# Kernel optimization log

Measured on AMD Instinct MI355X. Metric: run time of the kernel, lower is better.

Reference implementation:

```python
import jax, jax.numpy as jnp
import numpy as np

N, D, M, L, DEPTH, WIDTH, MPTS = 2048, 64, 2048, 16, 3, 128, 64
WIN = 2 * L + 1  # 33


def setup_inputs() -> dict:
    key = jax.random.key(0)
    ks = jax.random.split(key, 6)
    # xavier-normal-ish scales to keep sigmoids in a reasonable range
    s0 = float(np.sqrt(2.0 / (D + WIDTH)))
    s1 = float(np.sqrt(2.0 / (2 * WIDTH)))
    s2 = float(np.sqrt(2.0 / (WIDTH + WIN)))
    return {
        "u": jax.random.normal(ks[0], (MPTS, D), dtype=jnp.float32),
        "weight0": jax.random.normal(ks[1], (WIN, WIDTH, D), dtype=jnp.float32) * s0,
        "bias0": jnp.zeros((WIN, WIDTH, 1), dtype=jnp.float32),
        "weight": jax.random.normal(ks[2], (DEPTH - 1, WIN, WIDTH, WIDTH), dtype=jnp.float32) * s1,
        "bias": jnp.zeros((DEPTH - 1, WIN, WIDTH, 1), dtype=jnp.float32),
        "weight_final": jax.random.normal(ks[3], (M, WIN, WIDTH), dtype=jnp.float32) * s2,
        "bias_final": jnp.zeros((M, WIN, 1), dtype=jnp.float32),
        "xi": jax.random.normal(ks[4], (M, N + 2 * L), dtype=jnp.float32) * 0.1,
    }


def reference(u, weight0, bias0, weight, bias, weight_final, bias_final, xi):
    sig = jax.nn.sigmoid
    # first_step: shared per-frequency MLP stack
    u1 = sig(jnp.einsum('jkl,ml->jkm', weight0, u) + bias0)
    for i in range(weight.shape[0]):  # depth-1 hidden layers (small fixed count)
        u1 = sig(jnp.einsum('jkl,jlm->jkm', weight[i], u1) + bias[i])
    G = sig(jnp.einsum('ijk,jkm->ijm', weight_final, u1) + bias_final)
    # sliding-window weighted sum over spectral coeffs, vectorized as a 1D
    # cross-correlation: out[n, p] = sum_{m,j} xi[m, n+j] * G[m, j, p]
    kernel = jnp.transpose(G, (2, 0, 1))
    out = jax.lax.conv_general_dilated(
        xi[None],  # [1, M, N+2L]
        kernel,
        window_strides=(1,),
        padding='VALID',
        dimension_numbers=('NCH', 'OIH', 'NCH'),
    )  # [1, MPTS, N]
    return out[0].T  # [N, MPTS] == torch.cat over iter_prod
```

## Files before the change

### kernel.cpp

```cpp
#include <hip/hip_runtime.h>

#define WIN 33
#define WIDTH 128
#define MPTS 64
#define NN 2048
#define MM 2048
#define DD 64
#define NQ 2080

typedef __bf16 bf16x8 __attribute__((ext_vector_type(8)));
typedef float f32x4 __attribute__((ext_vector_type(4)));

__device__ __forceinline__ unsigned short f2bf(float x) {
  union { float f; unsigned int u; } v; v.f = x;
  unsigned int r = v.u + 0x7FFFu + ((v.u >> 16) & 1u);
  return (unsigned short)(r >> 16);
}
__device__ __forceinline__ float sigf(float x) { return 1.0f / (1.0f + __expf(-x)); }

__device__ __forceinline__ void gll16(const unsigned short* g, unsigned short* l) {
  __builtin_amdgcn_global_load_lds(
      (const __attribute__((address_space(1))) unsigned int*)g,
      (__attribute__((address_space(3))) unsigned int*)l, 16, 0, 0);
}

__global__ __launch_bounds__(256) void k_transpose(const float* __restrict__ xi,
                                                   unsigned short* __restrict__ xiT) {
  __shared__ float ts[64 * 37];
  int qb = blockIdx.x * 32;
  int mb = blockIdx.y * 64;
#pragma unroll
  for (int c = threadIdx.x; c < 512; c += 256) {
    int row = c >> 3, c8 = c & 7;
    float4 v = *(const float4*)&xi[(size_t)(mb + row) * NQ + qb + (c8 << 2)];
    ts[row * 37 + (c8 << 2) + 0] = v.x;
    ts[row * 37 + (c8 << 2) + 1] = v.y;
    ts[row * 37 + (c8 << 2) + 2] = v.z;
    ts[row * 37 + (c8 << 2) + 3] = v.w;
  }
  __syncthreads();
#pragma unroll
  for (int c = threadIdx.x; c < 512; c += 256) {
    int r = c >> 4, mq = c & 15;
    ushort4 h;
    h.x = f2bf(ts[(mq * 4 + 0) * 37 + r]);
    h.y = f2bf(ts[(mq * 4 + 1) * 37 + r]);
    h.z = f2bf(ts[(mq * 4 + 2) * 37 + r]);
    h.w = f2bf(ts[(mq * 4 + 3) * 37 + r]);
    *(ushort4*)&xiT[((size_t)blockIdx.y * NQ + (qb + r)) * 64 + (mq << 2)] = h;
  }
}

__global__ __launch_bounds__(256) void k_mlp(const float* __restrict__ u,
                                             const float* __restrict__ w0,
                                             const float* __restrict__ b0,
                                             const float* __restrict__ w,
                                             const float* __restrict__ bias,
                                             unsigned short* __restrict__ u1bf) {
  constexpr int WS = 72;
  constexpr int AS = 136;
  __shared__ unsigned short ws[128 * WS];
  __shared__ unsigned short actA[64 * AS];
  __shared__ unsigned short actB[64 * AS];
  __shared__ float biass[128];
  int j = blockIdx.x;
  int tid = threadIdx.x;
  int wv = tid >> 6, lane = tid & 63, l15 = lane & 15, l4 = lane >> 4;

#pragma unroll
  for (int c = tid; c < 1024; c += 256) {
    int p = c >> 4, d4 = (c & 15) << 2;
    float4 v = *(const float4*)&u[(size_t)p * DD + d4];
    ushort4 h; h.x = f2bf(v.x); h.y = f2bf(v.y); h.z = f2bf(v.z); h.w = f2bf(v.w);
    *(ushort4*)&actA[p * AS + d4] = h;
  }
#pragma unroll
  for (int c = tid; c < 2048; c += 256) {
    int k = c >> 4, d4 = (c & 15) << 2;
    float4 v = *(const float4*)&w0[((size_t)j * 128 + k) * DD + d4];
    ushort4 h; h.x = f2bf(v.x); h.y = f2bf(v.y); h.z = f2bf(v.z); h.w = f2bf(v.w);
    *(ushort4*)&ws[k * WS + d4] = h;
  }
  if (tid < 128) biass[tid] = b0[j * 128 + tid];
  __syncthreads();

  {
    f32x4 acc[2][4] = {};
#pragma unroll
    for (int t = 0; t < 2; ++t) {
      int col = (t << 5) + (l4 << 3);
      bf16x8 a[2], b[4];
#pragma unroll
      for (int s = 0; s < 2; ++s)
        a[s] = *(const bf16x8*)&ws[(wv * 32 + s * 16 + l15) * WS + col];
#pragma unroll
      for (int q = 0; q < 4; ++q)
        b[q] = *(const bf16x8*)&actA[(q * 16 + l15) * AS + col];
#pragma unroll
      for (int s = 0; s < 2; ++s)
#pragma unroll
        for (int q = 0; q < 4; ++q)
          acc[s][q] = __builtin_amdgcn_mfma_f32_16x16x32_bf16(a[s], b[q], acc[s][q], 0, 0, 0);
    }
#pragma unroll
    for (int s = 0; s < 2; ++s)
#pragma unroll
      for (int q = 0; q < 4; ++q) {
        int p = q * 16 + l15;
#pragma unroll
        for (int r = 0; r < 4; ++r) {
          int k = wv * 32 + s * 16 + (l4 << 2) + r;
          actB[p * AS + k] = f2bf(sigf(acc[s][q][r] + biass[k]));
        }
      }
  }

  unsigned short* ain = actB;
  unsigned short* aout = actA;
#pragma unroll
  for (int i = 0; i < 2; ++i) {
    f32x4 acc[2][4] = {};
    const float* wbase = w + ((size_t)i * WIN + j) * 128 * 128;
#pragma unroll
    for (int h = 0; h < 2; ++h) {
      __syncthreads();
#pragma unroll
      for (int c = tid; c < 2048; c += 256) {
        int k = c >> 4, d4 = (c & 15) << 2;
        float4 v = *(const float4*)&wbase[(size_t)k * 128 + h * 64 + d4];
        ushort4 hh; hh.x = f2bf(v.x); hh.y = f2bf(v.y); hh.z = f2bf(v.z); hh.w = f2bf(v.w);
        *(ushort4*)&ws[k * WS + d4] = hh;
      }
      if (h == 0 && tid < 128) biass[tid] = bias[((size_t)i * WIN + j) * 128 + tid];
      __syncthreads();
#pragma unroll
      for (int t = 0; t < 2; ++t) {
        int col = (t << 5) + (l4 << 3);
        bf16x8 a[2], b[4];
#pragma unroll
        for (int s = 0; s < 2; ++s)
          a[s] = *(const bf16x8*)&ws[(wv * 32 + s * 16 + l15) * WS + col];
#pragma unroll
        for (int q = 0; q < 4; ++q)
          b[q] = *(const bf16x8*)&ain[(q * 16 + l15) * AS + h * 64 + col];
#pragma unroll
        for (int s = 0; s < 2; ++s)
#pragma unroll
          for (int q = 0; q < 4; ++q)
            acc[s][q] = __builtin_amdgcn_mfma_f32_16x16x32_bf16(a[s], b[q], acc[s][q], 0, 0, 0);
      }
    }
#pragma unroll
    for (int s = 0; s < 2; ++s)
#pragma unroll
      for (int q = 0; q < 4; ++q) {
        int p = q * 16 + l15;
#pragma unroll
        for (int r = 0; r < 4; ++r) {
          int k = wv * 32 + s * 16 + (l4 << 2) + r;
          aout[p * AS + k] = f2bf(sigf(acc[s][q][r] + biass[k]));
        }
      }
    unsigned short* t2 = ain; ain = aout; aout = t2;
  }
  __syncthreads();
#pragma unroll
  for (int c = tid; c < 1024; c += 256) {
    int p = c >> 4, k8 = (c & 15) << 3;
    uint4 v = *(const uint4*)&ain[p * AS + k8];
    *(uint4*)&u1bf[((size_t)j * MPTS + p) * WIDTH + k8] = v;
  }
}

__global__ __launch_bounds__(256) void k_final(const float* __restrict__ wf,
                                               const float* __restrict__ bfin,
                                               const unsigned short* __restrict__ u1bf,
                                               unsigned short* __restrict__ Gt2) {
  constexpr int KP = 136;
  __shared__ unsigned short As[64 * KP];
  __shared__ unsigned short Bs[64 * KP];
  __shared__ float bfs[64];
  int bid = blockIdx.x;
  int j = bid >> 5;
  int m0 = (bid & 31) << 6;
#pragma unroll
  for (int c = threadIdx.x; c < 64 * 32; c += 256) {
    int row = c >> 5, f4 = c & 31;
    float4 v = *(const float4*)(wf + ((size_t)(m0 + row) * WIN + j) * WIDTH + (f4 << 2));
    ushort4 h;
    h.x = f2bf(v.x); h.y = f2bf(v.y); h.z = f2bf(v.z); h.w = f2bf(v.w);
    *(ushort4*)(&As[row * KP + (f4 << 2)]) = h;
  }
#pragma unroll
  for (int c = threadIdx.x; c < 64 * 16; c += 256) {
    int p = c >> 4, ch = c & 15;
    uint4 v = *(const uint4*)(u1bf + (size_t)(j * MPTS + p) * WIDTH + (ch << 3));
    *(uint4*)(&Bs[p * KP + (ch << 3)]) = v;
  }
  if (threadIdx.x < 64) bfs[threadIdx.x] = bfin[(size_t)(m0 + threadIdx.x) * WIN + j];
  __syncthreads();
  int wv = threadIdx.x >> 6, lane = threadIdx.x & 63;
  int l15 = lane & 15, l4 = lane >> 4;
  f32x4 acc[4] = {};
#pragma unroll
  for (int t = 0; t < 4; ++t) {
    int col = (t << 5) + (l4 << 3);
    bf16x8 a = *(const bf16x8*)(&As[(wv * 16 + l15) * KP + col]);
#pragma unroll
    for (int q = 0; q < 4; ++q) {
      bf16x8 bb = *(const bf16x8*)(&Bs[(q * 16 + l15) * KP + col]);
      acc[q] = __builtin_amdgcn_mfma_f32_16x16x32_bf16(a, bb, acc[q], 0, 0, 0);
    }
  }
  size_t region = (size_t)((bid & 31) << 1) + (wv >> 1);
  int g = ((wv & 1) << 1) + (l4 >> 1);
  int m8 = (l4 & 1) << 2;
  int mb = wv * 16 + (l4 << 2);
#pragma unroll
  for (int q = 0; q < 4; ++q) {
    int p = q * 16 + l15;
    float z0 = acc[q][0] + bfs[mb + 0];
    float z1 = acc[q][1] + bfs[mb + 1];
    float z2 = acc[q][2] + bfs[mb + 2];
    float z3 = acc[q][3] + bfs[mb + 3];
    ushort4 st;
    st.x = f2bf(sigf(z0)); st.y = f2bf(sigf(z1));
    st.z = f2bf(sigf(z2)); st.w = f2bf(sigf(z3));
    *(ushort4*)(&Gt2[region * 67584 + ((size_t)(j * 4 + g) * 64 + p) * 8 + m8]) = st;
  }
}

__global__ __launch_bounds__(256) void k_conv(const unsigned short* __restrict__ xiT,
                                              const unsigned short* __restrict__ Gt2,
                                              float* __restrict__ out) {
  extern __shared__ unsigned short lds[];
  unsigned short* As = lds;
  int bid = blockIdx.x;
  int mp = bid & 31;
  int n0 = (bid >> 5) << 7;
  int tid = threadIdx.x;
  int wv = tid >> 6, lane = tid & 63, l15 = lane & 15, l4 = lane >> 4;

  const unsigned short* Abase = xiT + (size_t)mp * (NQ * 64) + (size_t)n0 * 64;
#pragma unroll
  for (int k = 0; k < 5; ++k) {
    int instr = wv * 5 + k;
    int s = (instr << 6) + lane;
    int row = s >> 3;
    int c = (s & 7) ^ (row & 7);
    gll16(Abase + (size_t)row * 64 + (c << 3), As + (instr << 9));
  }

  constexpr int JBT[10]  = {0, 7, 14, 21, 28, 0, 7, 14, 21, 28};
  constexpr int CNTT[10] = {7, 7, 7, 7, 5, 7, 7, 7, 7, 5};
  constexpr int HFT[10]  = {0, 0, 0, 0, 0, 1, 1, 1, 1, 1};

  const unsigned short* Rb0 = Gt2 + (size_t)(mp << 1) * 67584;
  const unsigned short* Rb1 = Gt2 + (size_t)((mp << 1) + 1) * 67584;

  {
    const unsigned short* Bb = Rb0;
#pragma unroll
    for (int k = 0; k < 7; ++k) {
      int instr = wv * 7 + k;
      gll16(Bb + (((instr << 6) + lane) << 3), lds + 10240 + (instr << 9));
    }
  }

  f32x4 acc[2][4] = {};
#pragma unroll
  for (int t = 0; t < 10; ++t) {
    __syncthreads();
    if (t < 9) {
      const int jbn = JBT[t + 1], cntn = CNTT[t + 1];
      const unsigned short* Bb =
          (HFT[t + 1] ? Rb1 : Rb0) + ((size_t)jbn << 11);
      unsigned short* Bst = lds + 10240 + ((t + 1) & 1) * 14336;
#pragma unroll
      for (int k = 0; k < cntn; ++k) {
        int instr = wv * cntn + k;
        gll16(Bb + (((instr << 6) + lane) << 3), Bst + (instr << 9));
      }
    }
    {
      const int jb = JBT[t], cnt = CNTT[t], h4 = HFT[t] << 2;
      const unsigned short* Bs = lds + 10240 + (t & 1) * 14336;
      bf16x8 a[2], b[4];
#pragma unroll
      for (int s = 0; s < 2; ++s) {
        int row = wv * 32 + s * 16 + l15 + jb;
        a[s] = *(const bf16x8*)&As[row * 64 + (((h4 | l4) ^ (row & 7)) << 3)];
      }
#pragma unroll
      for (int q = 0; q < 4; ++q) {
        int slot = (l4 << 6) + (q << 4) + l15;
        b[q] = *(const bf16x8*)&Bs[slot << 3];
      }
#pragma unroll
      for (int jj = 0; jj < cnt; ++jj) {
        bf16x8 an[2], bn[4];
        if (jj < cnt - 1) {
#pragma unroll
          for (int s = 0; s < 2; ++s) {
            int row = wv * 32 + s * 16 + l15 + jb + jj + 1;
            an[s] = *(const bf16x8*)&As[row * 64 + (((h4 | l4) ^ (row & 7)) << 3)];
          }
#pragma unroll
          for (int q = 0; q < 4; ++q) {
            int slot = ((((jj + 1) << 2) + l4) << 6) + (q << 4) + l15;
            bn[q] = *(const bf16x8*)&Bs[slot << 3];
          }
        }
#pragma unroll
        for (int s = 0; s < 2; ++s)
#pragma unroll
          for (int q = 0; q < 4; ++q)
            acc[s][q] = __builtin_amdgcn_mfma_f32_16x16x32_bf16(a[s], b[q], acc[s][q], 0, 0, 0);
#pragma unroll
        for (int s = 0; s < 2; ++s) a[s] = an[s];
#pragma unroll
        for (int q = 0; q < 4; ++q) b[q] = bn[q];
      }
    }
  }
#pragma unroll
  for (int s = 0; s < 2; ++s)
#pragma unroll
    for (int q = 0; q < 4; ++q) {
      int nr = n0 + wv * 32 + s * 16 + (l4 << 2);
      int p = q * 16 + l15;
#pragma unroll
      for (int i = 0; i < 4; ++i)
        atomicAdd(&out[(size_t)(nr + i) * MPTS + p], acc[s][q][i]);
    }
}

extern "C" void kernel_launch(void* const* d_in, const int* in_sizes, int n_in,
                              void* d_out, int out_size, void* d_ws, size_t ws_size,
                              hipStream_t stream) {
  const float* u    = (const float*)d_in[0];
  const float* w0   = (const float*)d_in[1];
  const float* b0   = (const float*)d_in[2];
  const float* w    = (const float*)d_in[3];
  const float* bias = (const float*)d_in[4];
  const float* wf   = (const float*)d_in[5];
  const float* bfin = (const float*)d_in[6];
  const float* xi   = (const float*)d_in[7];
  float* out = (float*)d_out;
  char* ws = (char*)d_ws;
  unsigned short* xiT  = (unsigned short*)(ws);
  unsigned short* Gt2  = (unsigned short*)(ws + 8519680);
  unsigned short* u1bf = (unsigned short*)(ws + 17170432);

  hipFuncSetAttribute(reinterpret_cast<const void*>(&k_conv),
                      hipFuncAttributeMaxDynamicSharedMemorySize, 77824);

  hipMemsetAsync(out, 0, (size_t)out_size * sizeof(float), stream);
  k_transpose<<<dim3(65, 32), 256, 0, stream>>>(xi, xiT);
  k_mlp<<<WIN, 256, 0, stream>>>(u, w0, b0, w, bias, u1bf);
  k_final<<<33 * 32, 256, 0, stream>>>(wf, bfin, u1bf, Gt2);
  k_conv<<<512, 256, 77824, stream>>>(xiT, Gt2, out);
}
```

Measured before the change: 161.5 us.

## Fuse memset, xi transpose and MLP into one heterogeneous prep kernel

Replaces the output memset, the xi transpose kernel and the per-frequency MLP kernel with a single launch. Blocks 0-32 run the MLP, and the remaining blocks transpose xi to bf16 and zero the output. This removes two launch and serialization gaps and lets the small 33-block MLP overlap with the transpose work. In exchange, every block reserves the MLP's large dynamic shared memory, which may limit occupancy for the transpose blocks.

Result: faster. 153.3 us (-5.1%).

```diff
diff --git a/kernel.cpp b/kernel.cpp
--- a/kernel.cpp
+++ b/kernel.cpp
@@ -24,115 +24,48 @@
       (__attribute__((address_space(3))) unsigned int*)l, 16, 0, 0);
 }
 
-__global__ __launch_bounds__(256) void k_transpose(const float* __restrict__ xi,
-                                                   unsigned short* __restrict__ xiT) {
-  __shared__ float ts[64 * 37];
-  int qb = blockIdx.x * 32;
-  int mb = blockIdx.y * 64;
-#pragma unroll
-  for (int c = threadIdx.x; c < 512; c += 256) {
-    int row = c >> 3, c8 = c & 7;
-    float4 v = *(const float4*)&xi[(size_t)(mb + row) * NQ + qb + (c8 << 2)];
-    ts[row * 37 + (c8 << 2) + 0] = v.x;
-    ts[row * 37 + (c8 << 2) + 1] = v.y;
-    ts[row * 37 + (c8 << 2) + 2] = v.z;
-    ts[row * 37 + (c8 << 2) + 3] = v.w;
-  }
-  __syncthreads();
-#pragma unroll
-  for (int c = threadIdx.x; c < 512; c += 256) {
-    int r = c >> 4, mq = c & 15;
-    ushort4 h;
-    h.x = f2bf(ts[(mq * 4 + 0) * 37 + r]);
-    h.y = f2bf(ts[(mq * 4 + 1) * 37 + r]);
-    h.z = f2bf(ts[(mq * 4 + 2) * 37 + r]);
-    h.w = f2bf(ts[(mq * 4 + 3) * 37 + r]);
-    *(ushort4*)&xiT[((size_t)blockIdx.y * NQ + (qb + r)) * 64 + (mq << 2)] = h;
-  }
-}
-
-__global__ __launch_bounds__(256) void k_mlp(const float* __restrict__ u,
-                                             const float* __restrict__ w0,
-                                             const float* __restrict__ b0,
-                                             const float* __restrict__ w,
-                                             const float* __restrict__ bias,
-                                             unsigned short* __restrict__ u1bf) {
-  constexpr int WS = 72;
-  constexpr int AS = 136;
-  __shared__ unsigned short ws[128 * WS];
-  __shared__ unsigned short actA[64 * AS];
-  __shared__ unsigned short actB[64 * AS];
-  __shared__ float biass[128];
-  int j = blockIdx.x;
+__global__ __launch_bounds__(256) void k_prep(const float* __restrict__ xi,
+                                              unsigned short* __restrict__ xiT,
+                                              const float* __restrict__ u,
+                                              const float* __restrict__ w0,
+                                              const float* __restrict__ b0,
+                                              const float* __restrict__ w,
+                                              const float* __restrict__ bias,
+                                              unsigned short* __restrict__ u1bf,
+                                              float* __restrict__ out) {
+  extern __shared__ char smem[];
+  int bid = blockIdx.x;
   int tid = threadIdx.x;
-  int wv = tid >> 6, lane = tid & 63, l15 = lane & 15, l4 = lane >> 4;
-
-#pragma unroll
-  for (int c = tid; c < 1024; c += 256) {
-    int p = c >> 4, d4 = (c & 15) << 2;
-    float4 v = *(const float4*)&u[(size_t)p * DD + d4];
-    ushort4 h; h.x = f2bf(v.x); h.y = f2bf(v.y); h.z = f2bf(v.z); h.w = f2bf(v.w);
-    *(ushort4*)&actA[p * AS + d4] = h;
-  }
-#pragma unroll
-  for (int c = tid; c < 2048; c += 256) {
-    int k = c >> 4, d4 = (c & 15) << 2;
-    float4 v = *(const float4*)&w0[((size_t)j * 128 + k) * DD + d4];
-    ushort4 h; h.x = f2bf(v.x); h.y = f2bf(v.y); h.z = f2bf(v.z); h.w = f2bf(v.w);
-    *(ushort4*)&ws[k * WS + d4] = h;
-  }
-  if (tid < 128) biass[tid] = b0[j * 128 + tid];
-  __syncthreads();
-
-  {
-    f32x4 acc[2][4] = {};
-#pragma unroll
-    for (int t = 0; t < 2; ++t) {
-      int col = (t << 5) + (l4 << 3);
-      bf16x8 a[2], b[4];
-#pragma unroll
-      for (int s = 0; s < 2; ++s)
-        a[s] = *(const bf16x8*)&ws[(wv * 32 + s * 16 + l15) * WS + col];
-#pragma unroll
-      for (int q = 0; q < 4; ++q)
-        b[q] = *(const bf16x8*)&actA[(q * 16 + l15) * AS + col];
-#pragma unroll
-      for (int s = 0; s < 2; ++s)
-#pragma unroll
-        for (int q = 0; q < 4; ++q)
-          acc[s][q] = __builtin_amdgcn_mfma_f32_16x16x32_bf16(a[s], b[q], acc[s][q], 0, 0, 0);
-    }
-#pragma unroll
-    for (int s = 0; s < 2; ++s)
-#pragma unroll
-      for (int q = 0; q < 4; ++q) {
-        int p = q * 16 + l15;
-#pragma unroll
-        for (int r = 0; r < 4; ++r) {
-          int k = wv * 32 + s * 16 + (l4 << 2) + r;
-          actB[p * AS + k] = f2bf(sigf(acc[s][q][r] + biass[k]));
-        }
-      }
-  }
-
-  unsigned short* ain = actB;
-  unsigned short* aout = actA;
-#pragma unroll
-  for (int i = 0; i < 2; ++i) {
-    f32x4 acc[2][4] = {};
-    const float* wbase = w + ((size_t)i * WIN + j) * 128 * 128;
-#pragma unroll
-    for (int h = 0; h < 2; ++h) {
-      __syncthreads();
-#pragma unroll
-      for (int c = tid; c < 2048; c += 256) {
-        int k = c >> 4, d4 = (c & 15) << 2;
-        float4 v = *(const float4*)&wbase[(size_t)k * 128 + h * 64 + d4];
-        ushort4 hh; hh.x = f2bf(v.x); hh.y = f2bf(v.y); hh.z = f2bf(v.z); hh.w = f2bf(v.w);
-        *(ushort4*)&ws[k * WS + d4] = hh;
-      }
-      if (h == 0 && tid < 128) biass[tid] = bias[((size_t)i * WIN + j) * 128 + tid];
-      __syncthreads();
+
+  if (bid < 33) {
+    constexpr int WS = 72;
+    constexpr int AS = 136;
+    float* biass = (float*)smem;
+    unsigned short* ws   = (unsigned short*)(smem + 512);
+    unsigned short* actA = (unsigned short*)(smem + 18944);
+    unsigned short* actB = (unsigned short*)(smem + 36352);
+    int j = bid;
+    int wv = tid >> 6, lane = tid & 63, l15 = lane & 15, l4 = lane >> 4;
+
+#pragma unroll
+    for (int c = tid; c < 1024; c += 256) {
+      int p = c >> 4, d4 = (c & 15) << 2;
+      float4 v = *(const float4*)&u[(size_t)p * DD + d4];
+      ushort4 h; h.x = f2bf(v.x); h.y = f2bf(v.y); h.z = f2bf(v.z); h.w = f2bf(v.w);
+      *(ushort4*)&actA[p * AS + d4] = h;
+    }
+#pragma unroll
+    for (int c = tid; c < 2048; c += 256) {
+      int k = c >> 4, d4 = (c & 15) << 2;
+      float4 v = *(const float4*)&w0[((size_t)j * 128 + k) * DD + d4];
+      ushort4 h; h.x = f2bf(v.x); h.y = f2bf(v.y); h.z = f2bf(v.z); h.w = f2bf(v.w);
+      *(ushort4*)&ws[k * WS + d4] = h;
+    }
+    if (tid < 128) biass[tid] = b0[j * 128 + tid];
+    __syncthreads();
+
+    {
+      f32x4 acc[2][4] = {};
 #pragma unroll
       for (int t = 0; t < 2; ++t) {
         int col = (t << 5) + (l4 << 3);
@@ -142,33 +75,111 @@
           a[s] = *(const bf16x8*)&ws[(wv * 32 + s * 16 + l15) * WS + col];
 #pragma unroll
         for (int q = 0; q < 4; ++q)
-          b[q] = *(const bf16x8*)&ain[(q * 16 + l15) * AS + h * 64 + col];
+          b[q] = *(const bf16x8*)&actA[(q * 16 + l15) * AS + col];
 #pragma unroll
         for (int s = 0; s < 2; ++s)
 #pragma unroll
           for (int q = 0; q < 4; ++q)
             acc[s][q] = __builtin_amdgcn_mfma_f32_16x16x32_bf16(a[s], b[q], acc[s][q], 0, 0, 0);
       }
-    }
-#pragma unroll
-    for (int s = 0; s < 2; ++s)
-#pragma unroll
-      for (int q = 0; q < 4; ++q) {
-        int p = q * 16 + l15;
-#pragma unroll
-        for (int r = 0; r < 4; ++r) {
-          int k = wv * 32 + s * 16 + (l4 << 2) + r;
-          aout[p * AS + k] = f2bf(sigf(acc[s][q][r] + biass[k]));
-        }
-      }
-    unsigned short* t2 = ain; ain = aout; aout = t2;
-  }
-  __syncthreads();
-#pragma unroll
-  for (int c = tid; c < 1024; c += 256) {
-    int p = c >> 4, k8 = (c & 15) << 3;
-    uint4 v = *(const uint4*)&ain[p * AS + k8];
-    *(uint4*)&u1bf[((size_t)j * MPTS + p) * WIDTH + k8] = v;
+#pragma unroll
+      for (int s = 0; s < 2; ++s)
+#pragma unroll
+        for (int q = 0; q < 4; ++q) {
+          int p = q * 16 + l15;
+#pragma unroll
+          for (int r = 0; r < 4; ++r) {
+            int k = wv * 32 + s * 16 + (l4 << 2) + r;
+            actB[p * AS + k] = f2bf(sigf(acc[s][q][r] + biass[k]));
+          }
+        }
+    }
+
+    unsigned short* ain = actB;
+    unsigned short* aout = actA;
+#pragma unroll
+    for (int i = 0; i < 2; ++i) {
+      f32x4 acc[2][4] = {};
+      const float* wbase = w + ((size_t)i * WIN + j) * 128 * 128;
+#pragma unroll
+      for (int h = 0; h < 2; ++h) {
+        __syncthreads();
+#pragma unroll
+        for (int c = tid; c < 2048; c += 256) {
+          int k = c >> 4, d4 = (c & 15) << 2;
+          float4 v = *(const float4*)&wbase[(size_t)k * 128 + h * 64 + d4];
+          ushort4 hh; hh.x = f2bf(v.x); hh.y = f2bf(v.y); hh.z = f2bf(v.z); hh.w = f2bf(v.w);
+          *(ushort4*)&ws[k * WS + d4] = hh;
+        }
+        if (h == 0 && tid < 128) biass[tid] = bias[((size_t)i * WIN + j) * 128 + tid];
+        __syncthreads();
+#pragma unroll
+        for (int t = 0; t < 2; ++t) {
+          int col = (t << 5) + (l4 << 3);
+          bf16x8 a[2], b[4];
+#pragma unroll
+          for (int s = 0; s < 2; ++s)
+            a[s] = *(const bf16x8*)&ws[(wv * 32 + s * 16 + l15) * WS + col];
+#pragma unroll
+          for (int q = 0; q < 4; ++q)
+            b[q] = *(const bf16x8*)&ain[(q * 16 + l15) * AS + h * 64 + col];
+#pragma unroll
+          for (int s = 0; s < 2; ++s)
+#pragma unroll
+            for (int q = 0; q < 4; ++q)
+              acc[s][q] = __builtin_amdgcn_mfma_f32_16x16x32_bf16(a[s], b[q], acc[s][q], 0, 0, 0);
+        }
+      }
+#pragma unroll
+      for (int s = 0; s < 2; ++s)
+#pragma unroll
+        for (int q = 0; q < 4; ++q) {
+          int p = q * 16 + l15;
+#pragma unroll
+          for (int r = 0; r < 4; ++r) {
+            int k = wv * 32 + s * 16 + (l4 << 2) + r;
+            aout[p * AS + k] = f2bf(sigf(acc[s][q][r] + biass[k]));
+          }
+        }
+      unsigned short* t2 = ain; ain = aout; aout = t2;
+    }
+    __syncthreads();
+#pragma unroll
+    for (int c = tid; c < 1024; c += 256) {
+      int p = c >> 4, k8 = (c & 15) << 3;
+      uint4 v = *(const uint4*)&ain[p * AS + k8];
+      *(uint4*)&u1bf[((size_t)j * MPTS + p) * WIDTH + k8] = v;
+    }
+  } else {
+    float* ts = (float*)smem;
+    int t = bid - 33;
+    if (t < 512 && tid < 64) {
+      float4 z = {0.f, 0.f, 0.f, 0.f};
+      *(float4*)&out[((size_t)t << 8) + (tid << 2)] = z;
+    }
+    int qt = t % 65, mt = t / 65;
+    int qb = qt * 32;
+    int mb = mt * 64;
+#pragma unroll
+    for (int c = tid; c < 512; c += 256) {
+      int row = c >> 3, c8 = c & 7;
+      float4 v = *(const float4*)&xi[(size_t)(mb + row) * NQ + qb + (c8 << 2)];
+      ts[row * 37 + (c8 << 2) + 0] = v.x;
+      ts[row * 37 + (c8 << 2) + 1] = v.y;
+      ts[row * 37 + (c8 << 2) + 2] = v.z;
+      ts[row * 37 + (c8 << 2) + 3] = v.w;
+    }
+    __syncthreads();
+#pragma unroll
+    for (int c = tid; c < 512; c += 256) {
+      int r = c >> 4, mq = c & 15;
+      ushort4 h;
+      h.x = f2bf(ts[(mq * 4 + 0) * 37 + r]);
+      h.y = f2bf(ts[(mq * 4 + 1) * 37 + r]);
+      h.z = f2bf(ts[(mq * 4 + 2) * 37 + r]);
+      h.w = f2bf(ts[(mq * 4 + 3) * 37 + r]);
+      *(ushort4*)&xiT[((size_t)mt * NQ + (qb + r)) * 64 + (mq << 2)] = h;
+    }
   }
 }
 
@@ -352,12 +363,12 @@
   unsigned short* Gt2  = (unsigned short*)(ws + 8519680);
   unsigned short* u1bf = (unsigned short*)(ws + 17170432);
 
+  hipFuncSetAttribute(reinterpret_cast<const void*>(&k_prep),
+                      hipFuncAttributeMaxDynamicSharedMemorySize, 53760);
   hipFuncSetAttribute(reinterpret_cast<const void*>(&k_conv),
                       hipFuncAttributeMaxDynamicSharedMemorySize, 77824);
 
-  hipMemsetAsync(out, 0, (size_t)out_size * sizeof(float), stream);
-  k_transpose<<<dim3(65, 32), 256, 0, stream>>>(xi, xiT);
-  k_mlp<<<WIN, 256, 0, stream>>>(u, w0, b0, w, bias, u1bf);
+  k_prep<<<2113, 256, 53760, stream>>>(xi, xiT, u, w0, b0, w, bias, u1bf, out);
   k_final<<<33 * 32, 256, 0, stream>>>(wf, bfin, u1bf, Gt2);
   k_conv<<<512, 256, 77824, stream>>>(xiT, Gt2, out);
 }
```
